# Kernel tuning notes

Hardware: AMD Instinct MI355X
Metric: run time of the kernel (lower is better)

## Reference

```python
import jax, jax.numpy as jnp
import numpy as np

HIDDEN = 512
EPS = 1e-5  # BatchNorm1d default eps


def _ligru_layer(x, Ww, Wu, gamma, beta):
    # x: [T, B, F] time-major. Bidirectional: stack flipped copy along batch.
    x2 = jnp.concatenate([x, x[::-1]], axis=1)          # [T, 2B, F]
    w = jnp.einsum('tbf,gf->tbg', x2, Ww)               # [T, 2B, 2H]
    # BatchNorm over flattened (T*2B) rows, per feature (training-mode stats)
    mean = jnp.mean(w, axis=(0, 1))
    var = jnp.mean((w - mean) ** 2, axis=(0, 1))
    w = gamma * (w - mean) * jax.lax.rsqrt(var + EPS) + beta

    H = Wu.shape[1]
    h0 = jnp.zeros((w.shape[1], H), dtype=w.dtype)

    def step(h, wk):
        gates = wk + h @ Wu.T                            # [2B, 2H]
        at, zt = gates[:, :H], gates[:, H:]
        zt = jax.nn.sigmoid(zt)
        hcand = jax.nn.relu(at)                          # drop_mask == 1 (dropout=0)
        h = zt * h + (1.0 - zt) * hcand
        return h, h

    _, h = jax.lax.scan(step, h0, w)                     # [T, 2B, H]
    B = x.shape[1]
    h_f, h_b = h[:, :B], h[:, B:]
    return jnp.concatenate([h_f, h_b[::-1]], axis=2)     # [T, B, 2H]


def setup_inputs() -> dict:
    key = jax.random.key(0)
    ks = jax.random.split(key, 7)
    B, T, F, H = 16, 500, 240, HIDDEN
    x = jax.random.normal(ks[0], (B, T, F), dtype=jnp.float32)
    # layer 0: in=F, layer 1: in=2H (bidirectional output)
    Ww0 = jax.random.normal(ks[1], (2 * H, F), dtype=jnp.float32) / np.sqrt(F)
    Wu0 = jax.random.normal(ks[2], (2 * H, H), dtype=jnp.float32) / np.sqrt(H)
    Ww1 = jax.random.normal(ks[3], (2 * H, 2 * H), dtype=jnp.float32) / np.sqrt(2 * H)
    Wu1 = jax.random.normal(ks[4], (2 * H, H), dtype=jnp.float32) / np.sqrt(H)
    g0 = jnp.ones((2 * H,), jnp.float32)
    b0 = jnp.zeros((2 * H,), jnp.float32)
    g1 = jnp.ones((2 * H,), jnp.float32)
    b1 = jnp.zeros((2 * H,), jnp.float32)
    return {"x": x, "Ww0": Ww0, "Wu0": Wu0, "g0": g0, "b0": b0,
            "Ww1": Ww1, "Wu1": Wu1, "g1": g1, "b1": b1}


def reference(x, Ww0, Wu0, g0, b0, Ww1, Wu1, g1, b1):
    h = x.transpose(1, 0, 2)                             # [T, B, F]
    h = _ligru_layer(h, Ww0, Wu0, g0, b0)                # [T, B, 2H]
    h = _ligru_layer(h, Ww1, Wu1, g1, b1)                # [T, B, 2H]
    return h.transpose(1, 0, 2)                          # [B, T, 2H]
```

## Files before the change

### kernel.cpp

```cpp
#include <hip/hip_runtime.h>
#include <math.h>
#include <stdint.h>

#define TT 500
#define B2 32
#define FF 240
#define HH 512
#define G2 1024
#define MROWS (TT*B2)
#define REC_WGS 8
#define FLAG_STRIDE 16
#define FLAGS_PER_LAYER (TT*8*FLAG_STRIDE)

typedef __attribute__((ext_vector_type(8))) short bf16x8;
typedef __attribute__((ext_vector_type(4))) short bf16x4;
typedef __attribute__((ext_vector_type(4))) float f32x4;

typedef __attribute__((address_space(1))) const unsigned int GU32;
typedef __attribute__((address_space(3))) unsigned int LU32;

static __device__ __forceinline__ unsigned short f2bf(float f) {
    union { float f; unsigned u; } v; v.f = f;
    unsigned r = v.u + 0x7FFFu + ((v.u >> 16) & 1u);
    return (unsigned short)(r >> 16);
}

static __device__ __forceinline__ void gload_lds16(const void* g, void* l) {
    __builtin_amdgcn_global_load_lds((GU32*)g, (LU32*)l, 16, 0, 0);
}

__global__ void zero_cnt(unsigned int* cnt) {
    cnt[blockIdx.x * 256 + threadIdx.x] = 0u;
}

__global__ __launch_bounds__(256)
void cvt_a0(const float* __restrict__ x, unsigned short* __restrict__ A0)
{
    const int idx = blockIdx.x * 256 + threadIdx.x;
    const int m = idx >> 5;
    const int k = (idx & 31) * 8;
    const int t = m >> 5, b2 = m & 31;
    bf16x8 o = {0,0,0,0,0,0,0,0};
    if (k < FF) {
        const float* p = (b2 < 16)
            ? x + ((size_t)(b2 * TT + t)) * FF + k
            : x + ((size_t)((b2 - 16) * TT + (TT - 1 - t))) * FF + k;
        f32x4 a = *(const f32x4*)p;
        f32x4 b = *(const f32x4*)(p + 4);
        #pragma unroll
        for (int j = 0; j < 4; ++j) { o[j] = (short)f2bf(a[j]); o[4+j] = (short)f2bf(b[j]); }
    }
    *(bf16x8*)(A0 + (size_t)m * 256 + k) = o;
}

template<int Kin, int Kout>
__global__ __launch_bounds__(256)
void cvt_pad(const float* __restrict__ src, unsigned short* __restrict__ dst)
{
    const int idx = blockIdx.x * 256 + threadIdx.x;
    const int r = idx / (Kout / 8);
    const int k = (idx % (Kout / 8)) * 8;
    bf16x8 o = {0,0,0,0,0,0,0,0};
    if (k + 8 <= Kin) {
        f32x4 a = *(const f32x4*)(src + (size_t)r * Kin + k);
        f32x4 b = *(const f32x4*)(src + (size_t)r * Kin + k + 4);
        #pragma unroll
        for (int j = 0; j < 4; ++j) { o[j] = (short)f2bf(a[j]); o[4+j] = (short)f2bf(b[j]); }
    }
    *(bf16x8*)(dst + (size_t)r * Kout + k) = o;
}

template<int K>
__global__ __launch_bounds__(256, 2)
void mfma_gemm(const unsigned short* __restrict__ A,
               const unsigned short* __restrict__ B,
               float* __restrict__ C)
{
    __shared__ alignas(16) char As[16384];
    __shared__ alignas(16) char Bs[16384];
    const int tid = threadIdx.x;
    const int wv = tid >> 6, l = tid & 63, l15 = l & 15, lg = l >> 4;
    const int m0 = blockIdx.x * 128, n0 = blockIdx.y * 128;
    const int wr = wv >> 1, wc = wv & 1;
    f32x4 acc[4][4];
    #pragma unroll
    for (int i = 0; i < 4; ++i)
        #pragma unroll
        for (int j = 0; j < 4; ++j) acc[i][j] = (f32x4){0.f, 0.f, 0.f, 0.f};

    for (int ko = 0; ko < K; ko += 64) {
        #pragma unroll
        for (int i = 0; i < 4; ++i) {
            const int ch = tid + i * 256;
            const int row = ch >> 3, q = ch & 7;
            const int kb = (q * 16) ^ ((row & 7) << 4);
            gload_lds16(A + (size_t)(m0 + row) * K + ko + (kb >> 1), As + ch * 16);
            gload_lds16(B + (size_t)(n0 + row) * K + ko + (kb >> 1), Bs + ch * 16);
        }
        __syncthreads();
        #pragma unroll
        for (int ks = 0; ks < 2; ++ks) {
            bf16x8 af[4], bf[4];
            #pragma unroll
            for (int ib = 0; ib < 4; ++ib) {
                const int r = wr * 64 + ib * 16 + l15;
                const int sz = (r & 7) << 4;
                const int kb0 = ks * 64 + lg * 8;
                bf16x4 lo = *(const bf16x4*)(As + r * 128 + (kb0 ^ sz));
                bf16x4 hi = *(const bf16x4*)(As + r * 128 + ((kb0 + 32) ^ sz));
                bf16x8 f;
                f[0]=lo[0]; f[1]=lo[1]; f[2]=lo[2]; f[3]=lo[3];
                f[4]=hi[0]; f[5]=hi[1]; f[6]=hi[2]; f[7]=hi[3];
                af[ib] = f;
            }
            #pragma unroll
            for (int jb = 0; jb < 4; ++jb) {
                const int r = wc * 64 + jb * 16 + l15;
                const int sz = (r & 7) << 4;
                const int kb0 = ks * 64 + lg * 8;
                bf16x4 lo = *(const bf16x4*)(Bs + r * 128 + (kb0 ^ sz));
                bf16x4 hi = *(const bf16x4*)(Bs + r * 128 + ((kb0 + 32) ^ sz));
                bf16x8 f;
                f[0]=lo[0]; f[1]=lo[1]; f[2]=lo[2]; f[3]=lo[3];
                f[4]=hi[0]; f[5]=hi[1]; f[6]=hi[2]; f[7]=hi[3];
                bf[jb] = f;
            }
            #pragma unroll
            for (int ib = 0; ib < 4; ++ib)
                #pragma unroll
                for (int jb = 0; jb < 4; ++jb)
                    acc[ib][jb] = __builtin_amdgcn_mfma_f32_16x16x32_bf16(af[ib], bf[jb], acc[ib][jb], 0, 0, 0);
        }
        __syncthreads();
    }
    #pragma unroll
    for (int ib = 0; ib < 4; ++ib)
        #pragma unroll
        for (int jb = 0; jb < 4; ++jb)
            #pragma unroll
            for (int rr = 0; rr < 4; ++rr)
                C[(size_t)(m0 + wr * 64 + ib * 16 + lg * 4 + rr) * G2 +
                  (n0 + wc * 64 + jb * 16 + l15)] = acc[ib][jb][rr];
}

__global__ __launch_bounds__(256)
void stats_partial(const float* __restrict__ w, float* __restrict__ partS,
                   float* __restrict__ partQ)
{
    const int col = blockIdx.x * 256 + threadIdx.x;
    const int row0 = blockIdx.y * 128;
    float s = 0.f, q = 0.f;
    for (int r = 0; r < 128; ++r) {
        float v = w[(size_t)(row0 + r) * G2 + col];
        s += v; q += v * v;
    }
    partS[blockIdx.y * G2 + col] = s;
    partQ[blockIdx.y * G2 + col] = q;
}

__global__ __launch_bounds__(256)
void stats_final(const float* __restrict__ partS, const float* __restrict__ partQ,
                 const float* __restrict__ gamma, const float* __restrict__ beta,
                 float* __restrict__ scale, float* __restrict__ shift)
{
    const int col = blockIdx.x * 256 + threadIdx.x;
    float s = 0.f, q = 0.f;
    for (int i = 0; i < 125; ++i) { s += partS[i * G2 + col]; q += partQ[i * G2 + col]; }
    const float mean = s * (1.f / 16000.f);
    float var = q * (1.f / 16000.f) - mean * mean;
    var = fmaxf(var, 0.f);
    const float sc = gamma[col] * rsqrtf(var + 1e-5f);
    scale[col] = sc;
    shift[col] = beta[col] - mean * sc;
}

template<int LAYER>
__global__ __launch_bounds__(512, 2)
void rec_kernel(const float* __restrict__ w, const float* __restrict__ scale,
                const float* __restrict__ shift, const float* __restrict__ Wu,
                void* __restrict__ outp, unsigned short* __restrict__ hx,
                unsigned int* __restrict__ flags)
{
    __shared__ alignas(16) char hbuf[2][32768];

    const int g   = blockIdx.x;
    const int tid = threadIdx.x;
    const int wv  = tid >> 6;
    const int l   = tid & 63;
    const int c   = 4 * g + (wv >> 1);
    const int m   = wv & 1;
    const int l15 = l & 15;
    const int lg  = l >> 4;
    const int jcol = 16 * c + l15;
    const int jc   = jcol - 64 * g;

    bf16x8 bfa[16], bfz[16];
    {
        const float* pa = Wu + (size_t)jcol * HH;
        const float* pz = Wu + (size_t)(HH + jcol) * HH;
        #pragma unroll
        for (int ks = 0; ks < 16; ++ks) {
            f32x4 a0 = *(const f32x4*)(pa + ks * 32 + lg * 4);
            f32x4 a1 = *(const f32x4*)(pa + ks * 32 + lg * 4 + 16);
            f32x4 z0 = *(const f32x4*)(pz + ks * 32 + lg * 4);
            f32x4 z1 = *(const f32x4*)(pz + ks * 32 + lg * 4 + 16);
            bf16x8 fa, fz;
            #pragma unroll
            for (int j = 0; j < 4; ++j) {
                fa[j]     = (short)f2bf(a0[j]);
                fa[4 + j] = (short)f2bf(a1[j]);
                fz[j]     = (short)f2bf(z0[j]);
                fz[4 + j] = (short)f2bf(z1[j]);
            }
            bfa[ks] = fa; bfz[ks] = fz;
        }
    }
    const float scl_a = scale[jcol],      sh_a = shift[jcol];
    const float scl_z = scale[HH + jcol], sh_z = shift[HH + jcol];

    float hold[4] = {0.f, 0.f, 0.f, 0.f};

    for (int i = tid; i < 4096; i += 512) ((uint4*)hbuf)[i] = make_uint4(0, 0, 0, 0);
    __syncthreads();

    for (int t = 0; t < TT; ++t) {
        const int p = t & 1;

        float wa_[4], wz_[4];
        #pragma unroll
        for (int r = 0; r < 4; ++r) {
            const int b = m * 16 + lg * 4 + r;
            const float* wp = w + ((size_t)t * B2 + b) * G2 + jcol;
            wa_[r] = wp[0];
            wz_[r] = wp[HH];
        }

        if (t > 0) {
            if (wv == 0) {
                const unsigned int* fl = flags + (size_t)(t - 1) * 8 * FLAG_STRIDE;
                unsigned v = 1u;
                do {
                    if (l < 8)
                        v = __hip_atomic_load(fl + l * FLAG_STRIDE, __ATOMIC_RELAXED,
                                              __HIP_MEMORY_SCOPE_AGENT);
                    if (__any(v == 0)) __builtin_amdgcn_s_sleep(2); else break;
                } while (true);
            }
            __syncthreads();

            const unsigned long long* src =
                (const unsigned long long*)(hx + (size_t)(p ^ 1) * 16384);
            const int row = tid >> 4, hc = tid & 15;
            char* db = hbuf[p] + row * 1024;
            const int swz2 = (row & 7) << 4;
            unsigned long long vv[7];
            #pragma unroll
            for (int i = 0; i < 7; ++i) {
                const int sw = i + (i >= g);
                vv[i] = __hip_atomic_load(src + sw * 512 + row * 16 + hc,
                                          __ATOMIC_RELAXED, __HIP_MEMORY_SCOPE_AGENT);
            }
            #pragma unroll
            for (int i = 0; i < 7; ++i) {
                const int sw = i + (i >= g);
                *(unsigned long long*)(db + ((sw * 128 + hc * 8) ^ swz2)) = vv[i];
            }
            __syncthreads();
        }

        f32x4 aacc = {0.f, 0.f, 0.f, 0.f};
        f32x4 zacc = {0.f, 0.f, 0.f, 0.f};
        const int arow = m * 16 + l15;
        const char* rbase = hbuf[p] + arow * 1024;
        const int swz = (arow & 7) << 4;
        #pragma unroll
        for (int ks = 0; ks < 16; ++ks) {
            const int off0 = ks * 64 + lg * 8;
            bf16x4 h0 = *(const bf16x4*)(rbase + (off0 ^ swz));
            bf16x4 h1 = *(const bf16x4*)(rbase + ((off0 + 32) ^ swz));
            bf16x8 af;
            af[0] = h0[0]; af[1] = h0[1]; af[2] = h0[2]; af[3] = h0[3];
            af[4] = h1[0]; af[5] = h1[1]; af[6] = h1[2]; af[7] = h1[3];
            aacc = __builtin_amdgcn_mfma_f32_16x16x32_bf16(af, bfa[ks], aacc, 0, 0, 0);
            zacc = __builtin_amdgcn_mfma_f32_16x16x32_bf16(af, bfz[ks], zacc, 0, 0, 0);
        }

        unsigned short* dst = hx + (size_t)p * 16384 + (size_t)g * 2048;
        #pragma unroll
        for (int r = 0; r < 4; ++r) {
            const int b = m * 16 + lg * 4 + r;
            const float aval = scl_a * wa_[r] + sh_a + aacc[r];
            const float zval = scl_z * wz_[r] + sh_z + zacc[r];
            const float zt = 1.f / (1.f + __expf(-zval));
            const float hn = zt * hold[r] + (1.f - zt) * fmaxf(aval, 0.f);
            hold[r] = hn;
            const unsigned short hb = f2bf(hn);
            if (LAYER == 0) {
                unsigned short* A1 = (unsigned short*)outp;
                const int cc = jcol + (m == 0 ? 0 : HH);
                const int r1 = t * B2 + b;
                const int r2 = (TT - 1 - t) * B2 + (m == 0 ? b + 16 : b - 16);
                A1[(size_t)r1 * G2 + cc] = hb;
                A1[(size_t)r2 * G2 + cc] = hb;
            } else {
                float* po = (float*)outp;
                const int bb = (m == 0) ? b : b - 16;
                const int tt = (m == 0) ? t : (TT - 1 - t);
                po[((size_t)bb * TT + tt) * G2 + jcol + (m == 0 ? 0 : HH)] = hn;
            }
            if (t < TT - 1) {
                __hip_atomic_store(dst + b * 64 + jc, hb, __ATOMIC_RELAXED,
                                   __HIP_MEMORY_SCOPE_AGENT);
                *(unsigned short*)(hbuf[p ^ 1] + b * 1024 +
                                   ((jcol * 2) ^ ((b & 7) << 4))) = hb;
            }
        }
        if (t < TT - 1) {
            __syncthreads();
            if (tid == 0)
                __hip_atomic_fetch_add(flags + ((size_t)t * 8 + g) * FLAG_STRIDE, 1u,
                                       __ATOMIC_RELAXED, __HIP_MEMORY_SCOPE_AGENT);
        }
    }
}

extern "C" void kernel_launch(void* const* d_in, const int* in_sizes, int n_in,
                              void* d_out, int out_size, void* d_ws, size_t ws_size,
                              hipStream_t stream)
{
    const float* x   = (const float*)d_in[0];
    const float* Ww0 = (const float*)d_in[1];
    const float* Wu0 = (const float*)d_in[2];
    const float* g0  = (const float*)d_in[3];
    const float* b0  = (const float*)d_in[4];
    const float* Ww1 = (const float*)d_in[5];
    const float* Wu1 = (const float*)d_in[6];
    const float* g1  = (const float*)d_in[7];
    const float* b1  = (const float*)d_in[8];
    float* out = (float*)d_out;

    float* w     = (float*)d_ws;
    float* scr0  = w + (size_t)MROWS * G2;
    float* scr1  = scr0 + (size_t)TT * B2 * HH;
    float* partS = scr1 + (size_t)TT * B2 * HH;
    float* partQ = partS + 125 * G2;
    float* scale = partQ + 125 * G2;
    float* shift = scale + G2;
    unsigned int* flags = (unsigned int*)(shift + G2);
    unsigned short* hx  = (unsigned short*)(flags + 2 * FLAGS_PER_LAYER);

    unsigned short* A0b = (unsigned short*)scr0;
    unsigned short* Wwb = (unsigned short*)(scr0 + 3 * 1024 * 1024);
    unsigned short* A1b = (unsigned short*)scr1;

    const size_t needed = ((size_t)MROWS * G2 + 2 * (size_t)TT * B2 * HH +
                           2 * 125 * G2 + 2 * G2) * 4 +
                          (size_t)2 * FLAGS_PER_LAYER * 4 + 2 * 16384 * 2;
    if (ws_size < needed) return;

    zero_cnt<<<2 * FLAGS_PER_LAYER / 256, 256, 0, stream>>>(flags);

    cvt_a0<<<2000, 256, 0, stream>>>(x, A0b);
    cvt_pad<240, 256><<<128, 256, 0, stream>>>(Ww0, Wwb);
    mfma_gemm<256><<<dim3(125, 8), 256, 0, stream>>>(A0b, Wwb, w);
    stats_partial<<<dim3(4, 125), 256, 0, stream>>>(w, partS, partQ);
    stats_final<<<4, 256, 0, stream>>>(partS, partQ, g0, b0, scale, shift);
    rec_kernel<0><<<REC_WGS, 512, 0, stream>>>(w, scale, shift, Wu0, A1b, hx, flags);

    cvt_pad<1024, 1024><<<512, 256, 0, stream>>>(Ww1, Wwb);
    mfma_gemm<1024><<<dim3(125, 8), 256, 0, stream>>>(A1b, Wwb, w);
    stats_partial<<<dim3(4, 125), 256, 0, stream>>>(w, partS, partQ);
    stats_final<<<4, 256, 0, stream>>>(partS, partQ, g1, b1, scale, shift);
    rec_kernel<1><<<REC_WGS, 512, 0, stream>>>(w, scale, shift, Wu1, out, hx,
                                               flags + FLAGS_PER_LAYER);
}
```

Before: 2.980 ms.

## Replace per-step flag barrier with parity bits embedded in exchanged hidden-state words

The cross-workgroup handoff of the recurrent hidden state no longer uses separate counter flags plus a spin-wait and an extra barrier. Instead, each 64-bit exchange word carries a parity bit in its low bit (stolen from a bf16 mantissa LSB), and consumers spin directly on the data until every word shows the expected epoch. The goal is to remove a round trip and a workgroup barrier from every serial timestep. The cost is a slight precision loss on one bf16 element per word, plus reliance on relaxed atomic ordering of 64-bit stores.

```diff
diff --git a/kernel.cpp b/kernel.cpp
--- a/kernel.cpp
+++ b/kernel.cpp
@@ -9,12 +9,11 @@
 #define G2 1024
 #define MROWS (TT*B2)
 #define REC_WGS 8
-#define FLAG_STRIDE 16
-#define FLAGS_PER_LAYER (TT*8*FLAG_STRIDE)
 
 typedef __attribute__((ext_vector_type(8))) short bf16x8;
 typedef __attribute__((ext_vector_type(4))) short bf16x4;
 typedef __attribute__((ext_vector_type(4))) float f32x4;
+typedef unsigned long long u64;
 
 typedef __attribute__((address_space(1))) const unsigned int GU32;
 typedef __attribute__((address_space(3))) unsigned int LU32;
@@ -29,8 +28,8 @@
     __builtin_amdgcn_global_load_lds((GU32*)g, (LU32*)l, 16, 0, 0);
 }
 
-__global__ void zero_cnt(unsigned int* cnt) {
-    cnt[blockIdx.x * 256 + threadIdx.x] = 0u;
+__global__ void init_hx(u64* hx) {
+    hx[blockIdx.x * 256 + threadIdx.x] = 1ull;
 }
 
 __global__ __launch_bounds__(256)
@@ -178,8 +177,7 @@
 __global__ __launch_bounds__(512, 2)
 void rec_kernel(const float* __restrict__ w, const float* __restrict__ scale,
                 const float* __restrict__ shift, const float* __restrict__ Wu,
-                void* __restrict__ outp, unsigned short* __restrict__ hx,
-                unsigned int* __restrict__ flags)
+                void* __restrict__ outp, u64* __restrict__ hx)
 {
     __shared__ alignas(16) char hbuf[2][32768];
 
@@ -192,7 +190,6 @@
     const int l15 = l & 15;
     const int lg  = l >> 4;
     const int jcol = 16 * c + l15;
-    const int jc   = jcol - 64 * g;
 
     bf16x8 bfa[16], bfz[16];
     {
@@ -223,6 +220,9 @@
     for (int i = tid; i < 4096; i += 512) ((uint4*)hbuf)[i] = make_uint4(0, 0, 0, 0);
     __syncthreads();
 
+    const int row = tid >> 4, hc = tid & 15;
+    const int swzc = (row & 7) << 4;
+
     for (int t = 0; t < TT; ++t) {
         const int p = t & 1;
 
@@ -236,34 +236,27 @@
         }
 
         if (t > 0) {
-            if (wv == 0) {
-                const unsigned int* fl = flags + (size_t)(t - 1) * 8 * FLAG_STRIDE;
-                unsigned v = 1u;
-                do {
-                    if (l < 8)
-                        v = __hip_atomic_load(fl + l * FLAG_STRIDE, __ATOMIC_RELAXED,
-                                              __HIP_MEMORY_SCOPE_AGENT);
-                    if (__any(v == 0)) __builtin_amdgcn_s_sleep(2); else break;
-                } while (true);
-            }
-            __syncthreads();
-
-            const unsigned long long* src =
-                (const unsigned long long*)(hx + (size_t)(p ^ 1) * 16384);
-            const int row = tid >> 4, hc = tid & 15;
+            const u64* src = hx + (size_t)(p ^ 1) * 4096;
+            const u64 e = (u64)(((t - 1) >> 1) & 1);
+            u64 vv[7];
+            unsigned done = 0;
+            while (done != 0x7Fu) {
+                #pragma unroll
+                for (int i = 0; i < 7; ++i) {
+                    if (!(done & (1u << i))) {
+                        const int sw = i + (i >= g);
+                        u64 v = __hip_atomic_load(src + sw * 512 + row * 16 + hc,
+                                                  __ATOMIC_RELAXED,
+                                                  __HIP_MEMORY_SCOPE_AGENT);
+                        if ((v & 1ull) == e) { vv[i] = v; done |= 1u << i; }
+                    }
+                }
+            }
             char* db = hbuf[p] + row * 1024;
-            const int swz2 = (row & 7) << 4;
-            unsigned long long vv[7];
             #pragma unroll
             for (int i = 0; i < 7; ++i) {
                 const int sw = i + (i >= g);
-                vv[i] = __hip_atomic_load(src + sw * 512 + row * 16 + hc,
-                                          __ATOMIC_RELAXED, __HIP_MEMORY_SCOPE_AGENT);
-            }
-            #pragma unroll
-            for (int i = 0; i < 7; ++i) {
-                const int sw = i + (i >= g);
-                *(unsigned long long*)(db + ((sw * 128 + hc * 8) ^ swz2)) = vv[i];
+                *(u64*)(db + ((sw * 128 + hc * 8) ^ swzc)) = vv[i];
             }
             __syncthreads();
         }
@@ -285,7 +278,6 @@
             zacc = __builtin_amdgcn_mfma_f32_16x16x32_bf16(af, bfz[ks], zacc, 0, 0, 0);
         }
 
-        unsigned short* dst = hx + (size_t)p * 16384 + (size_t)g * 2048;
         #pragma unroll
         for (int r = 0; r < 4; ++r) {
             const int b = m * 16 + lg * 4 + r;
@@ -308,18 +300,19 @@
                 const int tt = (m == 0) ? t : (TT - 1 - t);
                 po[((size_t)bb * TT + tt) * G2 + jcol + (m == 0 ? 0 : HH)] = hn;
             }
-            if (t < TT - 1) {
-                __hip_atomic_store(dst + b * 64 + jc, hb, __ATOMIC_RELAXED,
-                                   __HIP_MEMORY_SCOPE_AGENT);
+            if (t < TT - 1)
                 *(unsigned short*)(hbuf[p ^ 1] + b * 1024 +
                                    ((jcol * 2) ^ ((b & 7) << 4))) = hb;
-            }
-        }
+        }
+
         if (t < TT - 1) {
             __syncthreads();
-            if (tid == 0)
-                __hip_atomic_fetch_add(flags + ((size_t)t * 8 + g) * FLAG_STRIDE, 1u,
-                                       __ATOMIC_RELAXED, __HIP_MEMORY_SCOPE_AGENT);
+            const u64 e = (u64)((t >> 1) & 1);
+            u64 v = *(const u64*)(hbuf[p ^ 1] + row * 1024 +
+                                  ((128 * g + hc * 8) ^ swzc));
+            v = (v & ~1ull) | e;
+            __hip_atomic_store(hx + (size_t)p * 4096 + g * 512 + row * 16 + hc, v,
+                               __ATOMIC_RELAXED, __HIP_MEMORY_SCOPE_AGENT);
         }
     }
 }
@@ -346,31 +339,29 @@
     float* partQ = partS + 125 * G2;
     float* scale = partQ + 125 * G2;
     float* shift = scale + G2;
-    unsigned int* flags = (unsigned int*)(shift + G2);
-    unsigned short* hx  = (unsigned short*)(flags + 2 * FLAGS_PER_LAYER);
+    u64* hx0 = (u64*)(shift + G2);
+    u64* hx1 = hx0 + 8192;
 
     unsigned short* A0b = (unsigned short*)scr0;
     unsigned short* Wwb = (unsigned short*)(scr0 + 3 * 1024 * 1024);
     unsigned short* A1b = (unsigned short*)scr1;
 
     const size_t needed = ((size_t)MROWS * G2 + 2 * (size_t)TT * B2 * HH +
-                           2 * 125 * G2 + 2 * G2) * 4 +
-                          (size_t)2 * FLAGS_PER_LAYER * 4 + 2 * 16384 * 2;
+                           2 * 125 * G2 + 2 * G2) * 4 + 16384 * 8;
     if (ws_size < needed) return;
 
-    zero_cnt<<<2 * FLAGS_PER_LAYER / 256, 256, 0, stream>>>(flags);
+    init_hx<<<64, 256, 0, stream>>>(hx0);
 
     cvt_a0<<<2000, 256, 0, stream>>>(x, A0b);
     cvt_pad<240, 256><<<128, 256, 0, stream>>>(Ww0, Wwb);
     mfma_gemm<256><<<dim3(125, 8), 256, 0, stream>>>(A0b, Wwb, w);
     stats_partial<<<dim3(4, 125), 256, 0, stream>>>(w, partS, partQ);
     stats_final<<<4, 256, 0, stream>>>(partS, partQ, g0, b0, scale, shift);
-    rec_kernel<0><<<REC_WGS, 512, 0, stream>>>(w, scale, shift, Wu0, A1b, hx, flags);
+    rec_kernel<0><<<REC_WGS, 512, 0, stream>>>(w, scale, shift, Wu0, A1b, hx0);
 
     cvt_pad<1024, 1024><<<512, 256, 0, stream>>>(Ww1, Wwb);
     mfma_gemm<1024><<<dim3(125, 8), 256, 0, stream>>>(A1b, Wwb, w);
     stats_partial<<<dim3(4, 125), 256, 0, stream>>>(w, partS, partQ);
     stats_final<<<4, 256, 0, stream>>>(partS, partQ, g1, b1, scale, shift);
-    rec_kernel<1><<<REC_WGS, 512, 0, stream>>>(w, scale, shift, Wu1, out, hx,
-                                               flags + FLAGS_PER_LAYER);
-}
+    rec_kernel<1><<<REC_WGS, 512, 0, stream>>>(w, scale, shift, Wu1, out, hx1);
+}
```

Result: slower. 3.965 ms (+33.1%).
